# Optimization experiments

Hardware: AMD Instinct MI355X
Metric: run time of the kernel (lower is better)

The kernel has to match this reference:

```python
import jax, jax.numpy as jnp
import numpy as np

T = 4096      # tokens (flattened batch*seq)
DIN = 2048    # input hidden dim
DQ = 2048     # q output dim
DKV = 2048    # per-head-group kv output dim (== DQ here, MHA)
NA = 4        # number of adapters (LoRA/delta models)
R = 16        # lora rank per q/k/v


def setup_inputs() -> dict:
    key = jax.random.key(0)
    ks = jax.random.split(key, 8)
    def rn(k, shape, scale):
        return jax.random.normal(k, shape, dtype=jnp.float32) * scale
    return {
        "x": rn(ks[0], (T, DIN), 1.0),
        "W_base": rn(ks[1], (DQ + 2 * DKV, DIN), DIN ** -0.5),
        "A_buffer_qkv": rn(ks[2], (NA, DIN, 3 * R), DIN ** -0.5),
        "B_buffer_q": rn(ks[3], (NA, R, DQ), R ** -0.5),
        "B_buffer_kv": rn(ks[4], (NA, R, 2 * DKV), R ** -0.5),
        "DeltaW_q": rn(ks[5], (NA, DIN, DQ), DIN ** -0.5),
        "DeltaW_kv": rn(ks[6], (NA, DIN, 2 * DKV), DIN ** -0.5),
        "weight_indices": jax.random.randint(ks[7], (T,), 0, NA, dtype=jnp.int32),
    }


def _ldmm(indices, x, A, B, D):
    """Per-token adapter-indexed (LoRA + dense delta) matmul.
    indices: [T] int, x: [T, din], A: [na, din, r], B: [na, r, dout], D: [na, din, dout].
    out[t] = (x[t] @ A[a]) @ B[a] + x[t] @ D[a]  with a = indices[t].
    Implemented as masked GEMMs over the small fixed adapter set.
    """
    na = A.shape[0]
    out = jnp.zeros((x.shape[0], B.shape[2]), dtype=x.dtype)
    for a in range(na):  # small fixed loop over adapters
        xa = jnp.where((indices == a)[:, None], x, jnp.zeros((), x.dtype))
        out = out + (xa @ A[a]) @ B[a] + xa @ D[a]
    return out


def reference(x, W_base, A_buffer_qkv, B_buffer_q, B_buffer_kv,
              DeltaW_q, DeltaW_kv, weight_indices):
    # base QKV projection (ColumnParallelLinear, no bias): [T, dq + 2*dkv]
    base = x @ W_base.T
    rank = A_buffer_qkv.shape[2] // 3
    b_dim_q = B_buffer_q.shape[2]
    b_dim_kv = B_buffer_kv.shape[2] // 2
    d_dim_kv = DeltaW_kv.shape[2] // 2
    for i in range(3):  # q, k, v slices
        if i == 0:
            o = _ldmm(weight_indices, x,
                      A_buffer_qkv[:, :, :rank], B_buffer_q, DeltaW_q)
            base = base.at[:, :b_dim_q].add(o)
        else:
            o = _ldmm(weight_indices, x,
                      A_buffer_qkv[:, :, i * rank:(i + 1) * rank],
                      B_buffer_kv[:, :, (i - 1) * b_dim_kv:i * b_dim_kv],
                      DeltaW_kv[:, :, (i - 1) * d_dim_kv:i * d_dim_kv])
            base = base.at[:, i * b_dim_kv:(i + 1) * b_dim_kv].add(o)
    return base
```

## Files before the change

### kernel.cpp

```cpp
#include <hip/hip_runtime.h>
#include <stdint.h>

#define T_TOK 4096
#define DIN   2048
#define DQ    2048
#define DKV   2048
#define NOUT  (DQ + 2*DKV)
#define NA    4
#define RLORA 16
#define BM    256
#define BN    256
#define MPAD  (T_TOK + NA*BM)
#define MTILES (MPAD/BM)
#define KX    (DIN + 64)
#define NKT   (KX/32)
#define KSPLIT 16
#define NTBLK (NOUT/BN)
#define NWG   (MTILES*NTBLK)

typedef unsigned short u16;
typedef __attribute__((ext_vector_type(8))) short short8;
typedef __attribute__((ext_vector_type(8))) u16 u16x8;
typedef __attribute__((ext_vector_type(4))) float f32x4;

__device__ __forceinline__ u16 f2bf(float f) {
  uint32_t u = __float_as_uint(f);
  u = (u + 0x7FFFu + ((u >> 16) & 1u)) >> 16;
  return (u16)u;
}
__device__ __forceinline__ float bf2f(u16 u) {
  return __uint_as_float(((uint32_t)u) << 16);
}

typedef __attribute__((address_space(3))) void lds_void;
typedef __attribute__((address_space(1))) void glb_void;

__device__ __forceinline__ void gl_lds16(const void* g, void* l) {
  __builtin_amdgcn_global_load_lds((const glb_void*)(uintptr_t)g,
                                   (lds_void*)(uint32_t)(uintptr_t)l, 16, 0, 0);
}

__global__ void prep_kernel(const int* __restrict__ widx,
                            int* __restrict__ tok,
                            int* __restrict__ tileAdapter) {
  __shared__ int cnt[256][NA];
  __shared__ int total[NA];
  __shared__ int pad_off[NA];
  const int tid = threadIdx.x;
  const int CH = T_TOK / 256;
  const int base = tid * CH;
  int c[NA] = {0, 0, 0, 0};
  for (int i = 0; i < CH; i++) c[widx[base + i]]++;
  for (int a = 0; a < NA; a++) cnt[tid][a] = c[a];
  __syncthreads();
  if (tid < NA) {
    int s = 0;
    for (int i = 0; i < 256; i++) { int v = cnt[i][tid]; cnt[i][tid] = s; s += v; }
    total[tid] = s;
  }
  __syncthreads();
  if (tid == 0) {
    int off = 0;
    for (int a = 0; a < NA; a++) {
      pad_off[a] = off;
      int ntile = (total[a] + BM - 1) / BM;
      for (int tl = 0; tl < ntile; tl++) tileAdapter[off / BM + tl] = a;
      off += ntile * BM;
    }
    for (int tl = off / BM; tl < MTILES; tl++) tileAdapter[tl] = -1;
  }
  __syncthreads();
  for (int i = tid; i < MPAD; i += 256) tok[i] = -1;
  __syncthreads();
  int myoff[NA];
  for (int a = 0; a < NA; a++) myoff[a] = pad_off[a] + cnt[tid][a];
  for (int i = 0; i < CH; i++) {
    int a = widx[base + i];
    tok[myoff[a]++] = base + i;
  }
}

__global__ void gather_kernel(const float* __restrict__ x,
                              const int* __restrict__ tok,
                              u16* __restrict__ Xg) {
  const int row = blockIdx.x;
  const int t = tok[row];
  const int tid = threadIdx.x;
  u16x8* dst = (u16x8*)(Xg + (size_t)row * KX);
  if (t < 0) {
    u16x8 z = {0, 0, 0, 0, 0, 0, 0, 0};
    dst[tid] = z;
    return;
  }
  const f32x4* src = (const f32x4*)(x + (size_t)t * DIN);
  f32x4 v0 = src[tid * 2];
  f32x4 v1 = src[tid * 2 + 1];
  u16x8 o;
  o[0] = f2bf(v0[0]); o[1] = f2bf(v0[1]); o[2] = f2bf(v0[2]); o[3] = f2bf(v0[3]);
  o[4] = f2bf(v1[0]); o[5] = f2bf(v1[1]); o[6] = f2bf(v1[2]); o[7] = f2bf(v1[3]);
  dst[tid] = o;
}

__global__ __launch_bounds__(256) void xa_partial_kernel(
    const u16* __restrict__ Xg, const float* __restrict__ A_qkv,
    const int* __restrict__ tileAdapter, float* __restrict__ Ppart) {
  const int ks = blockIdx.y;
  const int ad = tileAdapter[blockIdx.x >> 1];
  const int a = ad < 0 ? 0 : ad;
  const int kb = ks * (DIN / KSPLIT);
  const int tid = threadIdx.x;
  const int rg = tid >> 2;
  const int jg = tid & 3;
  const int r0 = blockIdx.x * 128 + rg * 2;
  const int j0 = jg * 12;
  __shared__ float ldsA[64][56];
  float acc[2][12];
  #pragma unroll
  for (int r = 0; r < 2; r++)
    #pragma unroll
    for (int j = 0; j < 12; j++) acc[r][j] = 0.f;

  for (int kc = 0; kc < 2; kc++) {
    const int kbase = kb + kc * 64;
    for (int i = tid; i < 64 * 48; i += 256) {
      int kk = i / 48, j = i - kk * 48;
      ldsA[kk][j] = A_qkv[((size_t)a * DIN + kbase + kk) * (3 * RLORA) + j];
    }
    __syncthreads();
    u16x8 xr[2][8];
    #pragma unroll
    for (int r = 0; r < 2; r++)
      #pragma unroll
      for (int q = 0; q < 8; q++)
        xr[r][q] = *(const u16x8*)(Xg + (size_t)(r0 + r) * KX + kbase + q * 8);
    #pragma unroll
    for (int q = 0; q < 8; q++) {
      #pragma unroll
      for (int e = 0; e < 8; e++) {
        const int kk = q * 8 + e;
        f32x4 a0 = *(const f32x4*)&ldsA[kk][j0];
        f32x4 a1 = *(const f32x4*)&ldsA[kk][j0 + 4];
        f32x4 a2 = *(const f32x4*)&ldsA[kk][j0 + 8];
        float x0 = bf2f(xr[0][q][e]);
        float x1 = bf2f(xr[1][q][e]);
        #pragma unroll
        for (int c = 0; c < 4; c++) {
          acc[0][c]     += x0 * a0[c];  acc[1][c]     += x1 * a0[c];
          acc[0][4 + c] += x0 * a1[c];  acc[1][4 + c] += x1 * a1[c];
          acc[0][8 + c] += x0 * a2[c];  acc[1][8 + c] += x1 * a2[c];
        }
      }
    }
    __syncthreads();
  }
  #pragma unroll
  for (int r = 0; r < 2; r++)
    #pragma unroll
    for (int j = 0; j < 12; j++)
      Ppart[((size_t)ks * MPAD + r0 + r) * 48 + j0 + j] = acc[r][j];
}

__global__ void xa_reduce_kernel(const float* __restrict__ Ppart,
                                 u16* __restrict__ Xg) {
  const int gid = blockIdx.x * 256 + threadIdx.x;
  const int row = gid >> 6, j = gid & 63;
  float s = 0.f;
  if (j < 48) {
    #pragma unroll
    for (int sp = 0; sp < KSPLIT; sp++)
      s += Ppart[((size_t)sp * MPAD + row) * 48 + j];
  }
  Xg[(size_t)row * KX + DIN + j] = f2bf(s);
}

__global__ __launch_bounds__(256) void weff2_kernel(
    const float* __restrict__ W_base,
    const float* __restrict__ DW_q, const float* __restrict__ DW_kv,
    u16* __restrict__ Weff) {
  const int k0 = blockIdx.x * 64;
  const int n0 = blockIdx.y * 64;
  const int tid = threadIdx.x;
  const int k8 = (tid & 7) * 8;
  __shared__ float ldsD[64][65];

  f32x4 wb[2][2];
  #pragma unroll
  for (int h = 0; h < 2; h++) {
    const int nn = h * 32 + (tid >> 3);
    const float* p = W_base + (size_t)(n0 + nn) * DIN + k0 + k8;
    wb[h][0] = *(const f32x4*)p;
    wb[h][1] = *(const f32x4*)(p + 4);
  }

  const int ldD  = (n0 < DQ) ? DQ : 2 * DKV;
  const int ncol = (n0 < DQ) ? n0 : n0 - DQ;
  const float* Dbase = (n0 < DQ) ? (DW_q + ncol) : (DW_kv + ncol);
  const size_t Dstride = (n0 < DQ) ? (size_t)DIN * DQ : (size_t)DIN * (2 * DKV);

  const int lkk = tid >> 6;
  const int lnn = tid & 63;

  float v[16];
  {
    const float* Dp = Dbase;
    #pragma unroll
    for (int j = 0; j < 16; j++)
      v[j] = Dp[(size_t)(k0 + lkk + 4 * j) * ldD + lnn];
  }

  for (int a = 0; a < NA; a++) {
    #pragma unroll
    for (int j = 0; j < 16; j++) ldsD[lkk + 4 * j][lnn] = v[j];
    if (a < NA - 1) {
      const float* Dp = Dbase + (size_t)(a + 1) * Dstride;
      #pragma unroll
      for (int j = 0; j < 16; j++)
        v[j] = Dp[(size_t)(k0 + lkk + 4 * j) * ldD + lnn];
    }
    __syncthreads();
    #pragma unroll
    for (int h = 0; h < 2; h++) {
      const int nn = h * 32 + (tid >> 3);
      u16x8 o;
      #pragma unroll
      for (int j = 0; j < 8; j++)
        o[j] = f2bf(wb[h][j >> 2][j & 3] + ldsD[k8 + j][nn]);
      *(u16x8*)(Weff + ((size_t)a * NOUT + n0 + nn) * KX + k0 + k8) = o;
    }
    __syncthreads();
  }
}

__global__ void wslots_kernel(const float* __restrict__ B_q,
                              const float* __restrict__ B_kv,
                              u16* __restrict__ Weff) {
  const int a = blockIdx.y;
  const int n = blockIdx.x * 256 + threadIdx.x;
  const int seg = n >> 11;
  u16 vals[64];
  #pragma unroll
  for (int j = 0; j < 64; j++) vals[j] = 0;
  if (seg == 0) {
    const float* Bp = B_q + ((size_t)a * RLORA) * DQ + n;
    #pragma unroll
    for (int r = 0; r < RLORA; r++) vals[r] = f2bf(Bp[(size_t)r * DQ]);
  } else if (seg == 1) {
    const float* Bp = B_kv + ((size_t)a * RLORA) * (2 * DKV) + (n - DQ);
    #pragma unroll
    for (int r = 0; r < RLORA; r++) vals[RLORA + r] = f2bf(Bp[(size_t)r * (2 * DKV)]);
  } else {
    const float* Bp = B_kv + ((size_t)a * RLORA) * (2 * DKV) + (n - DQ);
    #pragma unroll
    for (int r = 0; r < RLORA; r++) vals[2 * RLORA + r] = f2bf(Bp[(size_t)r * (2 * DKV)]);
  }
  u16* dst = Weff + ((size_t)a * NOUT + n) * KX + DIN;
  #pragma unroll
  for (int v = 0; v < 8; v++) *(u16x8*)(dst + v * 8) = *(u16x8*)(vals + v * 8);
}

#define BAR      asm volatile("s_barrier" ::: "memory")
#define WAITV(n) asm volatile("s_waitcnt vmcnt(" #n ")" ::: "memory")

#define ST(b, t) { \
  _Pragma("unroll") for (int j = 0; j < 4; ++j) { \
    gl_lds16(gAsrc + (size_t)(j * 64) * KX + (size_t)(t) * 32, \
             ldsu + (b)*8192 + j*2048 + tid*8); \
    gl_lds16(gBsrc + (size_t)(j * 64) * KX + (size_t)(t) * 32, \
             ldsu + 32768 + (b)*8192 + j*2048 + tid*8); } }

#define RD(b) { \
  _Pragma("unroll") for (int q = 0; q < 8; ++q) \
    af[q] = *(const short8*)(ldsc + (b)*16384 + (wm*128 + q*16)*64 + laneoff); \
  _Pragma("unroll") for (int q = 0; q < 8; ++q) \
    bf[q] = *(const short8*)(ldsc + 65536 + (b)*16384 + (wn*128 + q*16)*64 + laneoff); }

#define MM64 { \
  __builtin_amdgcn_s_setprio(1); \
  _Pragma("unroll") for (int q = 0; q < 8; ++q) \
  _Pragma("unroll") for (int r = 0; r < 8; ++r) \
    acc[q][r] = __builtin_amdgcn_mfma_f32_16x16x32_bf16( \
        af[q], bf[r], acc[q][r], 0, 0, 0); \
  __builtin_amdgcn_s_setprio(0); }

#define TILE_S(b, t) { WAITV(16); BAR; RD(b); ST(((b)+3)&3, (t)+3); MM64; }
#define TILE_N(b, W) { W; BAR; RD(b); MM64; }

__global__ __launch_bounds__(256, 1) void gemm4w_kernel(
    const u16* __restrict__ Xg, const u16* __restrict__ Weff,
    const int* __restrict__ tok, const int* __restrict__ tileAdapter,
    float* __restrict__ out) {
  __shared__ __align__(16) u16 Lds[65536];

  const int bid = blockIdx.x;
  const int lw = (bid & 7) * (NWG / 8) + (bid >> 3);
  const int pg  = lw / (2 * NTBLK);
  const int rem = lw % (2 * NTBLK);
  const int nt  = rem >> 1;
  const int mt  = pg * 2 + (rem & 1);
  const int a = tileAdapter[mt];
  if (a < 0) return;
  const int m0 = mt * BM, n0 = nt * BN;

  const int tid = threadIdx.x;
  const int l = tid & 63, w = tid >> 6;
  const int wm = w >> 1, wn = w & 1;
  const int fr = l & 15;
  const int laneoff = fr * 64 + ((((l >> 4) ^ ((fr >> 1) & 3))) << 4);

  const int srow = tid >> 2;
  const int scol = (((tid & 3) ^ ((tid >> 3) & 3))) * 8;
  const u16* gAsrc = Xg + (size_t)(m0 + srow) * KX + scol;
  const u16* gBsrc = Weff + ((size_t)a * NOUT + n0 + srow) * KX + scol;

  u16* ldsu = &Lds[0];
  const char* ldsc = (const char*)ldsu;

  f32x4 acc[8][8];
  #pragma unroll
  for (int i = 0; i < 8; i++)
    #pragma unroll
    for (int j = 0; j < 8; j++) acc[i][j] = (f32x4){0.f, 0.f, 0.f, 0.f};

  short8 af[8], bf[8];

  ST(0, 0); ST(1, 1); ST(2, 2);

  for (int p = 0; p < 15; ++p) {
    const int t4 = 4 * p;
    TILE_S(0, t4 + 0);
    TILE_S(1, t4 + 1);
    TILE_S(2, t4 + 2);
    TILE_S(3, t4 + 3);
  }
  TILE_S(0, 60);
  TILE_S(1, 61);
  TILE_S(2, 62);
  TILE_N(3, WAITV(16));
  TILE_N(0, WAITV(8));
  TILE_N(1, WAITV(0));

  #pragma unroll
  for (int mi = 0; mi < 8; ++mi) {
    const int rb = m0 + wm * 128 + mi * 16 + ((l >> 4) << 2);
    int tt[4];
    #pragma unroll
    for (int reg = 0; reg < 4; ++reg) tt[reg] = tok[rb + reg];
    #pragma unroll
    for (int ni = 0; ni < 8; ++ni) {
      const int col = n0 + wn * 128 + ni * 16 + fr;
      #pragma unroll
      for (int reg = 0; reg < 4; ++reg)
        if (tt[reg] >= 0) out[(size_t)tt[reg] * NOUT + col] = acc[mi][ni][reg];
    }
  }
}

__global__ void fallback_kernel(const float* __restrict__ x,
                                const float* __restrict__ W_base,
                                const float* __restrict__ A_qkv,
                                const float* __restrict__ B_q,
                                const float* __restrict__ B_kv,
                                const float* __restrict__ DW_q,
                                const float* __restrict__ DW_kv,
                                const int* __restrict__ widx,
                                float* __restrict__ out) {
  const int t = blockIdx.x;
  const int n = blockIdx.y * 256 + threadIdx.x;
  const int a = widx[t];
  __shared__ float xs[DIN];
  __shared__ float ys[3 * RLORA];
  for (int k = threadIdx.x; k < DIN; k += 256) xs[k] = x[(size_t)t * DIN + k];
  __syncthreads();
  if (threadIdx.x < 3 * RLORA) {
    float s = 0.f;
    const float* Ap = A_qkv + (size_t)a * DIN * (3 * RLORA) + threadIdx.x;
    for (int k = 0; k < DIN; k++) s += xs[k] * Ap[(size_t)k * (3 * RLORA)];
    ys[threadIdx.x] = s;
  }
  __syncthreads();
  const float* dcol; int ldD, roff; const float* bcol; int ldB;
  if (n < DQ) {
    dcol = DW_q + (size_t)a * DIN * DQ + n; ldD = DQ; roff = 0;
    bcol = B_q + (size_t)a * RLORA * DQ + n; ldB = DQ;
  } else {
    dcol = DW_kv + (size_t)a * DIN * (2 * DKV) + (n - DQ); ldD = 2 * DKV;
    roff = (n < 2 * DQ) ? RLORA : 2 * RLORA;
    bcol = B_kv + (size_t)a * RLORA * (2 * DKV) + (n - DQ); ldB = 2 * DKV;
  }
  const float* wrow = W_base + (size_t)n * DIN;
  float acc = 0.f;
  for (int k = 0; k < DIN; k++) acc += xs[k] * (wrow[k] + dcol[(size_t)k * ldD]);
  for (int r = 0; r < RLORA; r++) acc += ys[roff + r] * bcol[(size_t)r * ldB];
  out[(size_t)t * NOUT + n] = acc;
}

extern "C" void kernel_launch(void* const* d_in, const int* in_sizes, int n_in,
                              void* d_out, int out_size, void* d_ws, size_t ws_size,
                              hipStream_t stream) {
  const float* x      = (const float*)d_in[0];
  const float* W_base = (const float*)d_in[1];
  const float* A_qkv  = (const float*)d_in[2];
  const float* B_q    = (const float*)d_in[3];
  const float* B_kv   = (const float*)d_in[4];
  const float* DW_q   = (const float*)d_in[5];
  const float* DW_kv  = (const float*)d_in[6];
  const int*   widx   = (const int*)d_in[7];
  float* out = (float*)d_out;

  const size_t WEFF_BYTES = (size_t)NA * NOUT * KX * sizeof(u16);
  const size_t XG_BYTES   = (size_t)MPAD * KX * sizeof(u16);
  const size_t TOK_BYTES  = (size_t)MPAD * sizeof(int);
  const size_t TILE_BYTES = (size_t)MTILES * sizeof(int);
  const size_t need = WEFF_BYTES + XG_BYTES + TOK_BYTES + TILE_BYTES;

  if (ws_size < need) {
    fallback_kernel<<<dim3(T_TOK, NOUT / 256), 256, 0, stream>>>(
        x, W_base, A_qkv, B_q, B_kv, DW_q, DW_kv, widx, out);
    return;
  }

  char* ws = (char*)d_ws;
  u16* Weff = (u16*)ws;
  u16* Xg   = (u16*)(ws + WEFF_BYTES);
  int* tok  = (int*)(ws + WEFF_BYTES + XG_BYTES);
  int* tileAdapter = tok + MPAD;
  float* Ppart = (float*)ws;

  prep_kernel<<<1, 256, 0, stream>>>(widx, tok, tileAdapter);
  gather_kernel<<<MPAD, 256, 0, stream>>>(x, tok, Xg);
  xa_partial_kernel<<<dim3(MPAD / 128, KSPLIT), 256, 0, stream>>>(
      Xg, A_qkv, tileAdapter, Ppart);
  xa_reduce_kernel<<<MPAD * 64 / 256, 256, 0, stream>>>(Ppart, Xg);
  weff2_kernel<<<dim3(DIN / 64, NOUT / 64), 256, 0, stream>>>(
      W_base, DW_q, DW_kv, Weff);
  wslots_kernel<<<dim3(NOUT / 256, NA), 256, 0, stream>>>(B_q, B_kv, Weff);
  gemm4w_kernel<<<dim3(NWG), 256, 0, stream>>>(
      Xg, Weff, tok, tileAdapter, out);
}
```

Baseline: 279.3 us.

## Restructure GEMM to 512 threads with B fragments loaded directly from global

The main GEMM goes from 256 to 512 threads per block (8 waves in a 2x4 layout). Only the X tile is staged through LDS; each wave loads its weight-fragment operands straight from global memory into registers, double-buffered across k-steps. This halves LDS use and the per-wave accumulator count so two blocks can share a CU, trading weight reuse through LDS for higher occupancy. The delta-weight transpose kernel also switches to 16-byte vectorized global loads.

```diff
diff --git a/kernel.cpp b/kernel.cpp
--- a/kernel.cpp
+++ b/kernel.cpp
@@ -197,25 +197,25 @@
   const float* Dbase = (n0 < DQ) ? (DW_q + ncol) : (DW_kv + ncol);
   const size_t Dstride = (n0 < DQ) ? (size_t)DIN * DQ : (size_t)DIN * (2 * DKV);
 
-  const int lkk = tid >> 6;
-  const int lnn = tid & 63;
-
-  float v[16];
-  {
-    const float* Dp = Dbase;
-    #pragma unroll
-    for (int j = 0; j < 16; j++)
-      v[j] = Dp[(size_t)(k0 + lkk + 4 * j) * ldD + lnn];
-  }
+  const int lkk  = tid >> 4;
+  const int lnn4 = (tid & 15) * 4;
+
+  f32x4 v4[4];
+  #pragma unroll
+  for (int j = 0; j < 4; j++)
+    v4[j] = *(const f32x4*)(Dbase + (size_t)(k0 + lkk + 16 * j) * ldD + lnn4);
 
   for (int a = 0; a < NA; a++) {
     #pragma unroll
-    for (int j = 0; j < 16; j++) ldsD[lkk + 4 * j][lnn] = v[j];
+    for (int j = 0; j < 4; j++)
+      #pragma unroll
+      for (int c = 0; c < 4; c++)
+        ldsD[lkk + 16 * j][lnn4 + c] = v4[j][c];
     if (a < NA - 1) {
       const float* Dp = Dbase + (size_t)(a + 1) * Dstride;
       #pragma unroll
-      for (int j = 0; j < 16; j++)
-        v[j] = Dp[(size_t)(k0 + lkk + 4 * j) * ldD + lnn];
+      for (int j = 0; j < 4; j++)
+        v4[j] = *(const f32x4*)(Dp + (size_t)(k0 + lkk + 16 * j) * ldD + lnn4);
     }
     __syncthreads();
     #pragma unroll
@@ -261,35 +261,35 @@
 #define BAR      asm volatile("s_barrier" ::: "memory")
 #define WAITV(n) asm volatile("s_waitcnt vmcnt(" #n ")" ::: "memory")
 
-#define ST(b, t) { \
-  _Pragma("unroll") for (int j = 0; j < 4; ++j) { \
-    gl_lds16(gAsrc + (size_t)(j * 64) * KX + (size_t)(t) * 32, \
-             ldsu + (b)*8192 + j*2048 + tid*8); \
-    gl_lds16(gBsrc + (size_t)(j * 64) * KX + (size_t)(t) * 32, \
-             ldsu + 32768 + (b)*8192 + j*2048 + tid*8); } }
-
-#define RD(b) { \
+#define ST_A2(b, t) { \
+  gl_lds16(gAsrc + (size_t)(t) * 32, ldsu + (b)*8192 + tid * 8); \
+  gl_lds16(gAsrc + (size_t)128 * KX + (size_t)(t) * 32, \
+           ldsu + (b)*8192 + 4096 + tid * 8); }
+
+#define RD_A(b) { \
   _Pragma("unroll") for (int q = 0; q < 8; ++q) \
-    af[q] = *(const short8*)(ldsc + (b)*16384 + (wm*128 + q*16)*64 + laneoff); \
-  _Pragma("unroll") for (int q = 0; q < 8; ++q) \
-    bf[q] = *(const short8*)(ldsc + 65536 + (b)*16384 + (wn*128 + q*16)*64 + laneoff); }
-
-#define MM64 { \
+    af[q] = *(const short8*)(ldsc + (b)*16384 + (wm*128 + q*16 + fr)*64 + ck); }
+
+#define LDB(arr, t) { \
+  _Pragma("unroll") for (int q = 0; q < 4; ++q) \
+    arr[q] = *(const short8*)(gBf[q] + (size_t)(t) * 32); }
+
+#define MM64(arr) { \
   __builtin_amdgcn_s_setprio(1); \
   _Pragma("unroll") for (int q = 0; q < 8; ++q) \
-  _Pragma("unroll") for (int r = 0; r < 8; ++r) \
+  _Pragma("unroll") for (int r = 0; r < 4; ++r) \
     acc[q][r] = __builtin_amdgcn_mfma_f32_16x16x32_bf16( \
-        af[q], bf[r], acc[q][r], 0, 0, 0); \
+        af[q], arr[r], acc[q][r], 0, 0, 0); \
   __builtin_amdgcn_s_setprio(0); }
 
-#define TILE_S(b, t) { WAITV(16); BAR; RD(b); ST(((b)+3)&3, (t)+3); MM64; }
-#define TILE_N(b, W) { W; BAR; RD(b); MM64; }
-
-__global__ __launch_bounds__(256, 1) void gemm4w_kernel(
+#define TILE_S(b, t, USE, LOADSET) { \
+  WAITV(8); BAR; RD_A(b); ST_A2(((b)+3)&3, (t)+3); LDB(LOADSET, (t)+1); MM64(USE); }
+
+__global__ __launch_bounds__(512, 2) void gemm256b_kernel(
     const u16* __restrict__ Xg, const u16* __restrict__ Weff,
     const int* __restrict__ tok, const int* __restrict__ tileAdapter,
     float* __restrict__ out) {
-  __shared__ __align__(16) u16 Lds[65536];
+  __shared__ __align__(16) u16 Lds[4 * 8192];
 
   const int bid = blockIdx.x;
   const int lw = (bid & 7) * (NWG / 8) + (bid >> 3);
@@ -303,41 +303,47 @@
 
   const int tid = threadIdx.x;
   const int l = tid & 63, w = tid >> 6;
-  const int wm = w >> 1, wn = w & 1;
+  const int wm = w >> 2, wn = w & 3;
   const int fr = l & 15;
-  const int laneoff = fr * 64 + ((((l >> 4) ^ ((fr >> 1) & 3))) << 4);
+  const int ck = (((l >> 4) ^ ((fr >> 1) & 3)) << 4);
 
   const int srow = tid >> 2;
   const int scol = (((tid & 3) ^ ((tid >> 3) & 3))) * 8;
   const u16* gAsrc = Xg + (size_t)(m0 + srow) * KX + scol;
-  const u16* gBsrc = Weff + ((size_t)a * NOUT + n0 + srow) * KX + scol;
+
+  const u16* gBf[4];
+  #pragma unroll
+  for (int q = 0; q < 4; ++q)
+    gBf[q] = Weff + ((size_t)a * NOUT + n0 + wn * 64 + q * 16 + fr) * KX
+             + ((l >> 4) << 3);
 
   u16* ldsu = &Lds[0];
   const char* ldsc = (const char*)ldsu;
 
-  f32x4 acc[8][8];
+  f32x4 acc[8][4];
   #pragma unroll
   for (int i = 0; i < 8; i++)
     #pragma unroll
-    for (int j = 0; j < 8; j++) acc[i][j] = (f32x4){0.f, 0.f, 0.f, 0.f};
-
-  short8 af[8], bf[8];
-
-  ST(0, 0); ST(1, 1); ST(2, 2);
+    for (int j = 0; j < 4; j++) acc[i][j] = (f32x4){0.f, 0.f, 0.f, 0.f};
+
+  short8 af[8], bE[4], bO[4];
+
+  ST_A2(0, 0); ST_A2(1, 1); ST_A2(2, 2);
+  LDB(bE, 0);
 
   for (int p = 0; p < 15; ++p) {
     const int t4 = 4 * p;
-    TILE_S(0, t4 + 0);
-    TILE_S(1, t4 + 1);
-    TILE_S(2, t4 + 2);
-    TILE_S(3, t4 + 3);
-  }
-  TILE_S(0, 60);
-  TILE_S(1, 61);
-  TILE_S(2, 62);
-  TILE_N(3, WAITV(16));
-  TILE_N(0, WAITV(8));
-  TILE_N(1, WAITV(0));
+    TILE_S(0, t4 + 0, bE, bO);
+    TILE_S(1, t4 + 1, bO, bE);
+    TILE_S(2, t4 + 2, bE, bO);
+    TILE_S(3, t4 + 3, bO, bE);
+  }
+  TILE_S(0, 60, bE, bO);
+  TILE_S(1, 61, bO, bE);
+  TILE_S(2, 62, bE, bO);
+  { WAITV(8); BAR; RD_A(3); LDB(bE, 64); MM64(bO); }
+  { WAITV(6); BAR; RD_A(0); LDB(bO, 65); MM64(bE); }
+  { WAITV(4); BAR; RD_A(1);              MM64(bO); }
 
   #pragma unroll
   for (int mi = 0; mi < 8; ++mi) {
@@ -346,8 +352,8 @@
     #pragma unroll
     for (int reg = 0; reg < 4; ++reg) tt[reg] = tok[rb + reg];
     #pragma unroll
-    for (int ni = 0; ni < 8; ++ni) {
-      const int col = n0 + wn * 128 + ni * 16 + fr;
+    for (int ni = 0; ni < 4; ++ni) {
+      const int col = n0 + wn * 64 + ni * 16 + fr;
       #pragma unroll
       for (int reg = 0; reg < 4; ++reg)
         if (tt[reg] >= 0) out[(size_t)tt[reg] * NOUT + col] = acc[mi][ni][reg];
@@ -434,6 +440,6 @@
   weff2_kernel<<<dim3(DIN / 64, NOUT / 64), 256, 0, stream>>>(
       W_base, DW_q, DW_kv, Weff);
   wslots_kernel<<<dim3(NOUT / 256, NA), 256, 0, stream>>>(B_q, B_kv, Weff);
-  gemm4w_kernel<<<dim3(NWG), 256, 0, stream>>>(
+  gemm256b_kernel<<<dim3(NWG), 512, 0, stream>>>(
       Xg, Weff, tok, tileAdapter, out);
 }
```

Measured after the change: 344.5 us. 23.4% more time.
